# Optimization experiments

Measured on AMD Instinct MI355X. Metric: run time of the kernel, lower is better.

Reference implementation:

```python
import jax, jax.numpy as jnp
import numpy as np

NUM_HEADS = 8  # matches init_kwargs


def setup_inputs() -> dict:
    key = jax.random.key(0)
    ks = jax.random.split(key, 8)
    B, S, E = 2, 512, 256
    inp = {
        "query": jax.random.normal(ks[0], (B, S, E), dtype=jnp.float32),
        "key": jax.random.normal(ks[1], (B, S, E), dtype=jnp.float32),
        "value": jax.random.normal(ks[2], (B, S, E), dtype=jnp.float32),
        "relations": jax.random.randint(ks[3], (B, S, S), 0, 33, dtype=jnp.int64),
        "W_Q": jax.random.normal(ks[4], (E, E), dtype=jnp.float32) * (E ** -0.5),
        "W_K": jax.random.normal(ks[5], (E, E), dtype=jnp.float32) * (E ** -0.5),
        "W_V": jax.random.normal(ks[6], (E, E), dtype=jnp.float32) * (E ** -0.5),
        "rel_emb": jax.random.normal(ks[7], (33, E), dtype=jnp.float32),
    }
    return inp


def reference(query, key, value, relations, W_Q, W_K, W_V, rel_emb):
    B, S, E = query.shape
    H = NUM_HEADS
    D = E // H
    scale = 1.0 / np.sqrt(D).astype(np.float32)

    # Projections (torch Linear: x @ W.T), split heads -> [B,S,H,D]
    q = (query @ W_Q.T).reshape(B, S, H, D)
    k = (key @ W_K.T).reshape(B, S, H, D)
    v = (value @ W_V.T).reshape(B, S, H, D)

    # Per-pair relation bias r[b,i,j] -> [B,S,S,H,D]
    rh = rel_emb[relations].reshape(B, S, S, H, D)

    # Faithful to original indexing: scores[b,h,i,j] = q_i . (K_i + r_{ij}) / sqrt(D)
    # Split into the (j-independent) q.K_i diagonal term plus the relation term,
    # avoiding materializing the [B,S,S,H,D] K+r tensor.
    qk_diag = jnp.einsum("bihd,bihd->bhi", q, k)  # [B,H,S]
    scores = (qk_diag[..., None] + jnp.einsum("bihd,bijhd->bhij", q, rh)) * scale
    alpha = jax.nn.softmax(scores, axis=-1)  # [B,H,S,S]

    # z[b,i,h] = sum_j alpha[b,h,i,j] * (V_i + r_{ij})
    alpha_sum = jnp.einsum("bhij->bih", alpha)  # == 1, kept for faithfulness
    z = v * alpha_sum[..., None] + jnp.einsum("bhij,bijhd->bihd", alpha, rh)
    return z.reshape(B, S, E)
```

## Files before the change

kernel.cpp:

```cpp
#include <hip/hip_runtime.h>
#include <math.h>

namespace {
constexpr int E_  = 256;
constexpr int H_  = 8;
constexpr int D_  = 32;
constexpr int S_  = 512;
constexpr int B_  = 2;
constexpr int NR_ = 33;
constexpr int RC_ = 32;
constexpr int ROWS_ = B_ * S_;
}

using f32x4 = __attribute__((ext_vector_type(4))) float;
using s16x8 = __attribute__((ext_vector_type(8))) short;

__device__ inline unsigned pk_bf16(float a, float b) {
    unsigned ua = __float_as_uint(a); ua += 0x7FFFu + ((ua >> 16) & 1u);
    unsigned ub = __float_as_uint(b); ub += 0x7FFFu + ((ub >> 16) & 1u);
    return (ua >> 16) | (ub & 0xFFFF0000u);
}

__device__ inline int swz(int row, int kbyte) {
    return row * 128 + (kbyte ^ ((row & 7) << 4));
}

__global__ __launch_bounds__(256) void fused_kernel(
    const float* __restrict__ q_in, const float* __restrict__ k_in,
    const float* __restrict__ v_in,
    const float* __restrict__ WQ, const float* __restrict__ WK,
    const float* __restrict__ WV,
    const int*   __restrict__ relations,
    const float* __restrict__ rel_emb,
    float* __restrict__ out)
{
    __shared__ __align__(16) char  tiles[6][RC_ * 128];
    __shared__ __align__(16) float qkv_s[3][RC_][36];
    __shared__ __align__(16) float emb_s[NR_ * D_];
    __shared__ float qr_s[RC_ * NR_];
    __shared__ int   cnt_s[RC_ * NR_];
    __shared__ float qkd_s[RC_];

    const int t  = threadIdx.x;
    const int r0 = blockIdx.x * RC_;
    const int h  = blockIdx.y;
    const int c0 = h * D_;

    float4 pre[12];

    auto issue_loads = [&](int kt) {
        #pragma unroll
        for (int j = 0; j < 12; ++j) {
            const int tau = j >> 1;
            const int idx = t + 256 * (j & 1);
            const int row = idx >> 4;
            const int cf  = (idx & 15) * 4;
            const float* src = (tau == 0) ? q_in : (tau == 1) ? k_in
                             : (tau == 2) ? v_in : (tau == 3) ? WQ
                             : (tau == 4) ? WK   : WV;
            const int rb = (tau < 3) ? r0 : c0;
            pre[j] = *reinterpret_cast<const float4*>(
                &src[(size_t)(rb + row) * E_ + kt * 64 + cf]);
        }
    };
    auto write_tiles = [&]() {
        #pragma unroll
        for (int j = 0; j < 12; ++j) {
            const int tau = j >> 1;
            const int idx = t + 256 * (j & 1);
            const int row = idx >> 4;
            const int cb  = (idx & 15) * 8;
            *reinterpret_cast<uint2*>(tiles[tau] + swz(row, cb)) =
                make_uint2(pk_bf16(pre[j].x, pre[j].y), pk_bf16(pre[j].z, pre[j].w));
        }
    };

    for (int i = t; i < RC_ * NR_; i += 256) cnt_s[i] = 0;
    for (int g = t; g < NR_ * D_ / 4; g += 256) {
        const int r = g >> 3, d4 = (g & 7) * 4;
        *reinterpret_cast<float4*>(&emb_s[r * D_ + d4]) =
            *reinterpret_cast<const float4*>(&rel_emb[(size_t)r * E_ + c0 + d4]);
    }
    issue_loads(0);
    __syncthreads();

    {
        const int hrow = t >> 3, hl = t & 7;
        const int* relrow = relations + (size_t)(r0 + hrow) * S_;
        #pragma unroll
        for (int i = 0; i < 16; ++i) {
            const int4 rv = *reinterpret_cast<const int4*>(&relrow[hl * 4 + i * 32]);
            atomicAdd(&cnt_s[hrow * NR_ + rv.x], 1);
            atomicAdd(&cnt_s[hrow * NR_ + rv.y], 1);
            atomicAdd(&cnt_s[hrow * NR_ + rv.z], 1);
            atomicAdd(&cnt_s[hrow * NR_ + rv.w], 1);
        }
    }

    const int l  = t & 63;
    const int w  = t >> 6;
    const int mi = (w >> 1) * 16;
    const int ni = (w & 1) * 16;
    const int lr = l & 15;
    const int lk = (l >> 4) * 16;

    f32x4 accq = {}, acck = {}, accv = {};

    for (int kt = 0; kt < 4; ++kt) {
        write_tiles();
        __syncthreads();
        if (kt < 3) issue_loads(kt + 1);
        #pragma unroll
        for (int s = 0; s < 2; ++s) {
            const int kb = s * 64 + lk;
            const s16x8 aq = *reinterpret_cast<const s16x8*>(tiles[0] + swz(mi + lr, kb));
            const s16x8 ak = *reinterpret_cast<const s16x8*>(tiles[1] + swz(mi + lr, kb));
            const s16x8 av = *reinterpret_cast<const s16x8*>(tiles[2] + swz(mi + lr, kb));
            const s16x8 bq = *reinterpret_cast<const s16x8*>(tiles[3] + swz(ni + lr, kb));
            const s16x8 bk = *reinterpret_cast<const s16x8*>(tiles[4] + swz(ni + lr, kb));
            const s16x8 bv = *reinterpret_cast<const s16x8*>(tiles[5] + swz(ni + lr, kb));
            accq = __builtin_amdgcn_mfma_f32_16x16x32_bf16(aq, bq, accq, 0, 0, 0);
            acck = __builtin_amdgcn_mfma_f32_16x16x32_bf16(ak, bk, acck, 0, 0, 0);
            accv = __builtin_amdgcn_mfma_f32_16x16x32_bf16(av, bv, accv, 0, 0, 0);
        }
        __syncthreads();
    }

    #pragma unroll
    for (int j = 0; j < 4; ++j) {
        const int row = mi + (l >> 4) * 4 + j;
        const int col = ni + lr;
        qkv_s[0][row][col] = accq[j];
        qkv_s[1][row][col] = acck[j];
        qkv_s[2][row][col] = accv[j];
    }
    __syncthreads();

    const int erow = t >> 3, el = t & 7;

    {
        const f32x4 qv = *reinterpret_cast<const f32x4*>(&qkv_s[0][erow][el * 4]);
        const f32x4 kv = *reinterpret_cast<const f32x4*>(&qkv_s[1][erow][el * 4]);
        float p = qv[0]*kv[0] + qv[1]*kv[1] + qv[2]*kv[2] + qv[3]*kv[3];
        p += __shfl_xor(p, 1); p += __shfl_xor(p, 2); p += __shfl_xor(p, 4);
        if (el == 0) qkd_s[erow] = p;
    }

    for (int g = t; g < RC_ * NR_; g += 256) {
        const int row = g & 31, r = g >> 5;
        const f32x4* qp = reinterpret_cast<const f32x4*>(&qkv_s[0][row][0]);
        const f32x4* ep = reinterpret_cast<const f32x4*>(&emb_s[r * D_]);
        float s = 0.f;
        #pragma unroll
        for (int u = 0; u < 8; ++u) {
            const f32x4 a = qp[u], b = ep[u];
            s += a[0]*b[0] + a[1]*b[1] + a[2]*b[2] + a[3]*b[3];
        }
        qr_s[row * NR_ + r] = s;
    }
    __syncthreads();

    {
        constexpr float scale = 0.17677669529663687f;
        const float qkd = qkd_s[erow];
        float z[5], m = -1e30f;
        #pragma unroll
        for (int u = 0; u < 5; ++u) {
            const int r = el + 8 * u;
            z[u] = (r < NR_) ? (qkd + qr_s[erow * NR_ + r]) * scale : -1e30f;
            m = fmaxf(m, z[u]);
        }
        m = fmaxf(m, __shfl_xor(m, 1));
        m = fmaxf(m, __shfl_xor(m, 2));
        m = fmaxf(m, __shfl_xor(m, 4));
        float e[5], sum = 0.f;
        #pragma unroll
        for (int u = 0; u < 5; ++u) {
            const int r = el + 8 * u;
            e[u] = (r < NR_) ? (float)cnt_s[erow * NR_ + r] * __expf(z[u] - m) : 0.f;
            sum += e[u];
        }
        sum += __shfl_xor(sum, 1);
        sum += __shfl_xor(sum, 2);
        sum += __shfl_xor(sum, 4);
        const float inv = 1.0f / sum;
        #pragma unroll
        for (int u = 0; u < 5; ++u) {
            const int r = el + 8 * u;
            if (r < NR_) qr_s[erow * NR_ + r] = e[u] * inv;
        }
    }
    __syncthreads();

    {
        const int d0 = el * 4;
        f32x4 acc = *reinterpret_cast<const f32x4*>(&qkv_s[2][erow][d0]);
        #pragma unroll
        for (int r = 0; r < NR_; ++r) {
            const float wv = qr_s[erow * NR_ + r];
            const f32x4 ev = *reinterpret_cast<const f32x4*>(&emb_s[r * D_ + d0]);
            acc[0] += wv * ev[0]; acc[1] += wv * ev[1];
            acc[2] += wv * ev[2]; acc[3] += wv * ev[3];
        }
        *reinterpret_cast<f32x4*>(&out[(size_t)(r0 + erow) * E_ + c0 + d0]) = acc;
    }
}

extern "C" void kernel_launch(void* const* d_in, const int* in_sizes, int n_in,
                              void* d_out, int out_size, void* d_ws, size_t ws_size,
                              hipStream_t stream) {
    const float* query     = (const float*)d_in[0];
    const float* key       = (const float*)d_in[1];
    const float* value     = (const float*)d_in[2];
    const int*   relations = (const int*)  d_in[3];
    const float* W_Q       = (const float*)d_in[4];
    const float* W_K       = (const float*)d_in[5];
    const float* W_V       = (const float*)d_in[6];
    const float* rel_emb   = (const float*)d_in[7];
    float* out = (float*)d_out;

    dim3 grid(ROWS_ / RC_, H_);
    fused_kernel<<<grid, 256, 0, stream>>>(query, key, value, W_Q, W_K, W_V,
                                           relations, rel_emb, out);
}
```

Baseline: 14.66 us.

## Drop the key projection via softmax shift invariance and pipeline the projection loads

```diff
diff --git a/kernel.cpp b/kernel.cpp
--- a/kernel.cpp
+++ b/kernel.cpp
@@ -6,10 +6,9 @@
 constexpr int H_  = 8;
 constexpr int D_  = 32;
 constexpr int S_  = 512;
-constexpr int B_  = 2;
 constexpr int NR_ = 33;
 constexpr int RC_ = 32;
-constexpr int ROWS_ = B_ * S_;
+constexpr int ROWS_ = 1024;
 }
 
 using f32x4 = __attribute__((ext_vector_type(4))) float;
@@ -20,82 +19,91 @@
     unsigned ub = __float_as_uint(b); ub += 0x7FFFu + ((ub >> 16) & 1u);
     return (ua >> 16) | (ub & 0xFFFF0000u);
 }
+__device__ inline unsigned short bf16_1(float a) {
+    unsigned ua = __float_as_uint(a); ua += 0x7FFFu + ((ua >> 16) & 1u);
+    return (unsigned short)(ua >> 16);
+}
 
 __device__ inline int swz(int row, int kbyte) {
     return row * 128 + (kbyte ^ ((row & 7) << 4));
 }
 
+__device__ inline void bar_lgkm() {
+    asm volatile("s_waitcnt lgkmcnt(0)" ::: "memory");
+    __builtin_amdgcn_s_barrier();
+    __builtin_amdgcn_sched_barrier(0);
+}
+
 __global__ __launch_bounds__(256) void fused_kernel(
-    const float* __restrict__ q_in, const float* __restrict__ k_in,
-    const float* __restrict__ v_in,
-    const float* __restrict__ WQ, const float* __restrict__ WK,
-    const float* __restrict__ WV,
+    const float* __restrict__ q_in, const float* __restrict__ v_in,
+    const float* __restrict__ WQ,  const float* __restrict__ WV,
     const int*   __restrict__ relations,
     const float* __restrict__ rel_emb,
     float* __restrict__ out)
 {
-    __shared__ __align__(16) char  tiles[6][RC_ * 128];
-    __shared__ __align__(16) float qkv_s[3][RC_][36];
+    __shared__ __align__(16) char  tiles[4][RC_ * 128];
+    __shared__ __align__(16) float v_s[RC_][36];
+    __shared__ __align__(16) unsigned short qbf_s[RC_ * 32];
     __shared__ __align__(16) float emb_s[NR_ * D_];
-    __shared__ float qr_s[RC_ * NR_];
+    __shared__ __align__(16) unsigned short ebf_s[48 * 32];
+    __shared__ float qr_s[RC_][52];
     __shared__ int   cnt_s[RC_ * NR_];
-    __shared__ float qkd_s[RC_];
 
     const int t  = threadIdx.x;
     const int r0 = blockIdx.x * RC_;
     const int h  = blockIdx.y;
     const int c0 = h * D_;
 
-    float4 pre[12];
-
-    auto issue_loads = [&](int kt) {
-        #pragma unroll
-        for (int j = 0; j < 12; ++j) {
+    float4 pre[16];
+    auto issue = [&](int kt, int buf) {
+        #pragma unroll
+        for (int j = 0; j < 8; ++j) {
             const int tau = j >> 1;
             const int idx = t + 256 * (j & 1);
             const int row = idx >> 4;
             const int cf  = (idx & 15) * 4;
-            const float* src = (tau == 0) ? q_in : (tau == 1) ? k_in
-                             : (tau == 2) ? v_in : (tau == 3) ? WQ
-                             : (tau == 4) ? WK   : WV;
-            const int rb = (tau < 3) ? r0 : c0;
-            pre[j] = *reinterpret_cast<const float4*>(
+            const float* src = (tau == 0) ? q_in : (tau == 1) ? v_in
+                             : (tau == 2) ? WQ   : WV;
+            const int rb = (tau < 2) ? r0 : c0;
+            pre[buf * 8 + j] = *reinterpret_cast<const float4*>(
                 &src[(size_t)(rb + row) * E_ + kt * 64 + cf]);
         }
     };
-    auto write_tiles = [&]() {
-        #pragma unroll
-        for (int j = 0; j < 12; ++j) {
+    auto wtiles = [&](int buf) {
+        #pragma unroll
+        for (int j = 0; j < 8; ++j) {
             const int tau = j >> 1;
             const int idx = t + 256 * (j & 1);
             const int row = idx >> 4;
             const int cb  = (idx & 15) * 8;
+            const float4 p = pre[buf * 8 + j];
             *reinterpret_cast<uint2*>(tiles[tau] + swz(row, cb)) =
-                make_uint2(pk_bf16(pre[j].x, pre[j].y), pk_bf16(pre[j].z, pre[j].w));
+                make_uint2(pk_bf16(p.x, p.y), pk_bf16(p.z, p.w));
         }
     };
 
+    issue(0, 0);
+    issue(1, 1);
+    const int hrow = t >> 3, hl = t & 7;
+    int4 rel[16];
+    {
+        const int* relrow = relations + (size_t)(r0 + hrow) * S_;
+        #pragma unroll
+        for (int i = 0; i < 16; ++i)
+            rel[i] = *reinterpret_cast<const int4*>(&relrow[hl * 4 + i * 32]);
+    }
     for (int i = t; i < RC_ * NR_; i += 256) cnt_s[i] = 0;
     for (int g = t; g < NR_ * D_ / 4; g += 256) {
         const int r = g >> 3, d4 = (g & 7) * 4;
-        *reinterpret_cast<float4*>(&emb_s[r * D_ + d4]) =
-            *reinterpret_cast<const float4*>(&rel_emb[(size_t)r * E_ + c0 + d4]);
-    }
-    issue_loads(0);
-    __syncthreads();
-
-    {
-        const int hrow = t >> 3, hl = t & 7;
-        const int* relrow = relations + (size_t)(r0 + hrow) * S_;
-        #pragma unroll
-        for (int i = 0; i < 16; ++i) {
-            const int4 rv = *reinterpret_cast<const int4*>(&relrow[hl * 4 + i * 32]);
-            atomicAdd(&cnt_s[hrow * NR_ + rv.x], 1);
-            atomicAdd(&cnt_s[hrow * NR_ + rv.y], 1);
-            atomicAdd(&cnt_s[hrow * NR_ + rv.z], 1);
-            atomicAdd(&cnt_s[hrow * NR_ + rv.w], 1);
-        }
-    }
+        const float4 ev = *reinterpret_cast<const float4*>(
+            &rel_emb[(size_t)r * E_ + c0 + d4]);
+        *reinterpret_cast<float4*>(&emb_s[r * D_ + d4]) = ev;
+        *reinterpret_cast<uint2*>(&ebf_s[r * 32 + d4]) =
+            make_uint2(pk_bf16(ev.x, ev.y), pk_bf16(ev.z, ev.w));
+    }
+    for (int i = t; i < (48 - NR_) * 32 / 2; i += 256)
+        reinterpret_cast<unsigned*>(ebf_s + NR_ * 32)[i] = 0;
+    bar_lgkm();
 
     const int l  = t & 63;
     const int w  = t >> 6;
@@ -104,70 +112,73 @@
     const int lr = l & 15;
     const int lk = (l >> 4) * 16;
 
-    f32x4 accq = {}, acck = {}, accv = {};
-
+    f32x4 accq = {}, accv = {};
+
+    #pragma unroll
     for (int kt = 0; kt < 4; ++kt) {
-        write_tiles();
-        __syncthreads();
-        if (kt < 3) issue_loads(kt + 1);
+        wtiles(kt & 1);
+        if (kt < 2) issue(kt + 2, kt & 1);
+        bar_lgkm();
         #pragma unroll
         for (int s = 0; s < 2; ++s) {
             const int kb = s * 64 + lk;
             const s16x8 aq = *reinterpret_cast<const s16x8*>(tiles[0] + swz(mi + lr, kb));
-            const s16x8 ak = *reinterpret_cast<const s16x8*>(tiles[1] + swz(mi + lr, kb));
-            const s16x8 av = *reinterpret_cast<const s16x8*>(tiles[2] + swz(mi + lr, kb));
-            const s16x8 bq = *reinterpret_cast<const s16x8*>(tiles[3] + swz(ni + lr, kb));
-            const s16x8 bk = *reinterpret_cast<const s16x8*>(tiles[4] + swz(ni + lr, kb));
-            const s16x8 bv = *reinterpret_cast<const s16x8*>(tiles[5] + swz(ni + lr, kb));
+            const s16x8 av = *reinterpret_cast<const s16x8*>(tiles[1] + swz(mi + lr, kb));
+            const s16x8 bq = *reinterpret_cast<const s16x8*>(tiles[2] + swz(ni + lr, kb));
+            const s16x8 bv = *reinterpret_cast<const s16x8*>(tiles[3] + swz(ni + lr, kb));
             accq = __builtin_amdgcn_mfma_f32_16x16x32_bf16(aq, bq, accq, 0, 0, 0);
-            acck = __builtin_amdgcn_mfma_f32_16x16x32_bf16(ak, bk, acck, 0, 0, 0);
             accv = __builtin_amdgcn_mfma_f32_16x16x32_bf16(av, bv, accv, 0, 0, 0);
         }
-        __syncthreads();
+        #pragma unroll
+        for (int i = 0; i < 4; ++i) {
+            const int4 rv = rel[kt * 4 + i];
+            atomicAdd(&cnt_s[hrow * NR_ + rv.x], 1);
+            atomicAdd(&cnt_s[hrow * NR_ + rv.y], 1);
+            atomicAdd(&cnt_s[hrow * NR_ + rv.z], 1);
+            atomicAdd(&cnt_s[hrow * NR_ + rv.w], 1);
+        }
+        bar_lgkm();
     }
 
     #pragma unroll
     for (int j = 0; j < 4; ++j) {
         const int row = mi + (l >> 4) * 4 + j;
         const int col = ni + lr;
-        qkv_s[0][row][col] = accq[j];
-        qkv_s[1][row][col] = acck[j];
-        qkv_s[2][row][col] = accv[j];
-    }
-    __syncthreads();
+        v_s[row][col] = accv[j];
+        qbf_s[row * 32 + col] = bf16_1(accq[j]);
+    }
+    bar_lgkm();
+
+    {
+        const int kq = (l >> 4) * 8;
+        const int Hh = w >> 1;
+        const int G  = w & 1;
+        const s16x8 afr = *reinterpret_cast<const s16x8*>(&qbf_s[(Hh * 16 + lr) * 32 + kq]);
+        const s16x8 bfr = *reinterpret_cast<const s16x8*>(&ebf_s[(G  * 16 + lr) * 32 + kq]);
+        f32x4 r1 = {};
+        r1 = __builtin_amdgcn_mfma_f32_16x16x32_bf16(afr, bfr, r1, 0, 0, 0);
+        #pragma unroll
+        for (int j = 0; j < 4; ++j)
+            qr_s[Hh * 16 + (l >> 4) * 4 + j][G * 16 + lr] = r1[j];
+        if ((w & 1) == 0) {
+            const s16x8 bf2 = *reinterpret_cast<const s16x8*>(&ebf_s[(32 + lr) * 32 + kq]);
+            f32x4 r2 = {};
+            r2 = __builtin_amdgcn_mfma_f32_16x16x32_bf16(afr, bf2, r2, 0, 0, 0);
+            #pragma unroll
+            for (int j = 0; j < 4; ++j)
+                qr_s[Hh * 16 + (l >> 4) * 4 + j][32 + lr] = r2[j];
+        }
+    }
+    bar_lgkm();
 
     const int erow = t >> 3, el = t & 7;
-
-    {
-        const f32x4 qv = *reinterpret_cast<const f32x4*>(&qkv_s[0][erow][el * 4]);
-        const f32x4 kv = *reinterpret_cast<const f32x4*>(&qkv_s[1][erow][el * 4]);
-        float p = qv[0]*kv[0] + qv[1]*kv[1] + qv[2]*kv[2] + qv[3]*kv[3];
-        p += __shfl_xor(p, 1); p += __shfl_xor(p, 2); p += __shfl_xor(p, 4);
-        if (el == 0) qkd_s[erow] = p;
-    }
-
-    for (int g = t; g < RC_ * NR_; g += 256) {
-        const int row = g & 31, r = g >> 5;
-        const f32x4* qp = reinterpret_cast<const f32x4*>(&qkv_s[0][row][0]);
-        const f32x4* ep = reinterpret_cast<const f32x4*>(&emb_s[r * D_]);
-        float s = 0.f;
-        #pragma unroll
-        for (int u = 0; u < 8; ++u) {
-            const f32x4 a = qp[u], b = ep[u];
-            s += a[0]*b[0] + a[1]*b[1] + a[2]*b[2] + a[3]*b[3];
-        }
-        qr_s[row * NR_ + r] = s;
-    }
-    __syncthreads();
-
     {
         constexpr float scale = 0.17677669529663687f;
-        const float qkd = qkd_s[erow];
         float z[5], m = -1e30f;
         #pragma unroll
         for (int u = 0; u < 5; ++u) {
             const int r = el + 8 * u;
-            z[u] = (r < NR_) ? (qkd + qr_s[erow * NR_ + r]) * scale : -1e30f;
+            z[u] = (r < NR_) ? qr_s[erow][r] * scale : -1e30f;
             m = fmaxf(m, z[u]);
         }
         m = fmaxf(m, __shfl_xor(m, 1));
@@ -187,17 +198,17 @@
         #pragma unroll
         for (int u = 0; u < 5; ++u) {
             const int r = el + 8 * u;
-            if (r < NR_) qr_s[erow * NR_ + r] = e[u] * inv;
-        }
-    }
-    __syncthreads();
+            if (r < NR_) qr_s[erow][r] = e[u] * inv;
+        }
+    }
+    bar_lgkm();
 
     {
         const int d0 = el * 4;
-        f32x4 acc = *reinterpret_cast<const f32x4*>(&qkv_s[2][erow][d0]);
+        f32x4 acc = *reinterpret_cast<const f32x4*>(&v_s[erow][d0]);
         #pragma unroll
         for (int r = 0; r < NR_; ++r) {
-            const float wv = qr_s[erow * NR_ + r];
+            const float wv = qr_s[erow][r];
             const f32x4 ev = *reinterpret_cast<const f32x4*>(&emb_s[r * D_ + d0]);
             acc[0] += wv * ev[0]; acc[1] += wv * ev[1];
             acc[2] += wv * ev[2]; acc[3] += wv * ev[3];
@@ -210,16 +221,14 @@
                               void* d_out, int out_size, void* d_ws, size_t ws_size,
                               hipStream_t stream) {
     const float* query     = (const float*)d_in[0];
-    const float* key       = (const float*)d_in[1];
     const float* value     = (const float*)d_in[2];
     const int*   relations = (const int*)  d_in[3];
     const float* W_Q       = (const float*)d_in[4];
-    const float* W_K       = (const float*)d_in[5];
     const float* W_V       = (const float*)d_in[6];
     const float* rel_emb   = (const float*)d_in[7];
     float* out = (float*)d_out;
 
     dim3 grid(ROWS_ / RC_, H_);
-    fused_kernel<<<grid, 256, 0, stream>>>(query, key, value, W_Q, W_K, W_V,
+    fused_kernel<<<grid, 256, 0, stream>>>(query, value, W_Q, W_V,
                                            relations, rel_emb, out);
 }
```

New measurement: 12.49 us. -14.8%, faster.
